# Optimization experiments

Hardware: AMD Instinct MI355X
Metric: run time of the kernel (lower is better)

Reference implementation:

```python
import jax, jax.numpy as jnp
import numpy as np

B = 2          # batch
L = 2048       # seq len
D_MODEL = 1024
D_INNER = 2 * D_MODEL   # expand = 2
D_STATE = 16
D_CONV = 4
DT_RANK = D_MODEL // 16  # 64


def setup_inputs() -> dict:
    key = jax.random.key(0)
    kx, kf, kb = jax.random.split(key, 3)
    d = {"x": jax.random.normal(kx, (B, L, D_MODEL), jnp.float32)}
    for pre, k in (("f_", kf), ("b_", kb)):
        kk = jax.random.split(k, 6)
        d[pre + "in_proj_w"] = jax.random.normal(kk[0], (2 * D_INNER, D_MODEL), jnp.float32) * 0.02
        d[pre + "conv_w"] = jax.random.normal(kk[1], (D_INNER, 1, D_CONV), jnp.float32) * 0.2
        d[pre + "conv_b"] = jnp.zeros((D_INNER,), jnp.float32)
        d[pre + "x_proj_w"] = jax.random.normal(kk[2], (DT_RANK + 2 * D_STATE, D_INNER), jnp.float32) * 0.02
        d[pre + "dt_proj_w"] = jax.random.normal(kk[3], (D_INNER, DT_RANK), jnp.float32) * 0.02
        # dt bias init so softplus(bias) ~ dt in [exp(-4), exp(-2)] range (mamba-style)
        d[pre + "dt_proj_b"] = jax.random.uniform(kk[4], (D_INNER,), jnp.float32, minval=-4.0, maxval=-2.0)
        # S4D-real init: A = -[1..d_state]
        d[pre + "A_log"] = jnp.log(jnp.broadcast_to(jnp.arange(1, D_STATE + 1, dtype=jnp.float32), (D_INNER, D_STATE)))
        d[pre + "D"] = jnp.ones((D_INNER,), jnp.float32)
        d[pre + "out_proj_w"] = jax.random.normal(kk[5], (D_MODEL, D_INNER), jnp.float32) * 0.02
    return d


def _silu(x):
    return x * jax.nn.sigmoid(x)


def _selective_scan(u, dt, A, Bm, Cm, Dp):
    # u, dt: [B, L, d_inner]; Bm, Cm: [B, L, d_state]; A: [d_inner, d_state]; Dp: [d_inner]
    def step(h, inp):
        u_t, dt_t, B_t, C_t = inp                       # [B,d], [B,d], [B,n], [B,n]
        dA = jnp.exp(dt_t[..., None] * A)               # [B, d, n]  (ZOH discretization)
        dBu = dt_t[..., None] * B_t[:, None, :] * u_t[..., None]
        h = dA * h + dBu                                # [B, d, n]
        y = jnp.einsum('bdn,bn->bd', h, C_t)            # [B, d]
        return h, y

    h0 = jnp.zeros((u.shape[0], A.shape[0], A.shape[1]), u.dtype)
    xs = (jnp.swapaxes(u, 0, 1), jnp.swapaxes(dt, 0, 1),
          jnp.swapaxes(Bm, 0, 1), jnp.swapaxes(Cm, 0, 1))
    _, ys = jax.lax.scan(step, h0, xs)                  # ys: [L, B, d_inner]
    return jnp.swapaxes(ys, 0, 1) + u * Dp              # skip connection D*u


def _mamba(x, in_proj_w, conv_w, conv_b, x_proj_w, dt_proj_w, dt_proj_b, A_log, Dp, out_proj_w):
    # x: [B, L, d_model]
    xz = x @ in_proj_w.T                                # [B, L, 2*d_inner]
    xi, z = jnp.split(xz, 2, axis=-1)
    # depthwise causal conv1d, kernel D_CONV, output truncated to L (left pad)
    xc = jax.lax.conv_general_dilated(
        jnp.swapaxes(xi, 1, 2), conv_w, (1,), [(D_CONV - 1, 0)],
        dimension_numbers=('NCH', 'OIH', 'NCH'), feature_group_count=D_INNER)
    xi = _silu(jnp.swapaxes(xc, 1, 2) + conv_b)         # [B, L, d_inner]
    x_dbl = xi @ x_proj_w.T                             # [B, L, dt_rank + 2*d_state]
    dt, Bm, Cm = jnp.split(x_dbl, [DT_RANK, DT_RANK + D_STATE], axis=-1)
    dt = jax.nn.softplus(dt @ dt_proj_w.T + dt_proj_b)  # [B, L, d_inner]
    A = -jnp.exp(A_log)                                 # [d_inner, d_state]
    y = _selective_scan(xi, dt, A, Bm, Cm, Dp)
    y = y * _silu(z)                                    # gated
    return y @ out_proj_w.T                             # [B, L, d_model]


def reference(x,
              f_in_proj_w, f_conv_w, f_conv_b, f_x_proj_w, f_dt_proj_w, f_dt_proj_b, f_A_log, f_D, f_out_proj_w,
              b_in_proj_w, b_conv_w, b_conv_b, b_x_proj_w, b_dt_proj_w, b_dt_proj_b, b_A_log, b_D, b_out_proj_w):
    h_fwd = _mamba(x, f_in_proj_w, f_conv_w, f_conv_b, f_x_proj_w,
                   f_dt_proj_w, f_dt_proj_b, f_A_log, f_D, f_out_proj_w)
    h_bwd = _mamba(jnp.flip(x, axis=1), b_in_proj_w, b_conv_w, b_conv_b, b_x_proj_w,
                   b_dt_proj_w, b_dt_proj_b, b_A_log, b_D, b_out_proj_w)
    h_bwd = jnp.flip(h_bwd, axis=1)
    return jnp.concatenate([h_fwd, h_bwd], axis=-1)     # [B, L, 2*d_model]
```

## Files before the change

### kernel.cpp

```cpp
#include <hip/hip_runtime.h>

#define BB 2
#define LL 2048
#define DM 1024
#define DI 2048
#define NTOK (BB*LL)
#define NC 64
#define CL (LL/NC)
#define NCH (BB*DI)

typedef __bf16 bf16x8 __attribute__((ext_vector_type(8)));
typedef float f32x4 __attribute__((ext_vector_type(4)));
typedef int i32x4 __attribute__((ext_vector_type(4)));

#define LOG2E 1.44269504088896340736f

__device__ __forceinline__ float siluf(float x){ return x / (1.f + __expf(-x)); }
__device__ __forceinline__ float softplusf(float x){
  if (x > 20.f) return x;
  return log1pf(__expf(x));
}
__device__ __forceinline__ unsigned short f2bf(float f){
  unsigned int u = __builtin_bit_cast(unsigned int, f);
  u += 0x7fffu + ((u >> 16) & 1u);
  return (unsigned short)(u >> 16);
}
__device__ __forceinline__ float bf2f(unsigned short u){
  return __builtin_bit_cast(float, (unsigned int)u << 16);
}
template<typename CT>
__device__ __forceinline__ void st_ct(CT* p, float v){
  if constexpr (sizeof(CT)==2) *p = (CT)f2bf(v); else *p = (CT)v;
}

__device__ __forceinline__ void gl_lds16(const unsigned short* g, unsigned short* l){
  __builtin_amdgcn_global_load_lds(
      (const __attribute__((address_space(1))) void*)g,
      (__attribute__((address_space(3))) void*)l, 16, 0, 0);
}

#define SEG0 4096
#define SEG1 8192
#define SEG2 512
#define SEG3 256
#define SEG4 4096
#define CAST_BLOCKS (SEG0+SEG1+SEG2+SEG3+SEG4)

__device__ __forceinline__ void cast4(const float* src, unsigned short* dst){
  float4 v = *reinterpret_cast<const float4*>(src);
  ushort4 o; o.x=f2bf(v.x); o.y=f2bf(v.y); o.z=f2bf(v.z); o.w=f2bf(v.w);
  *reinterpret_cast<ushort4*>(dst) = o;
}

__global__ __launch_bounds__(256) void k_cast_all(
    const float* __restrict__ x,
    const float* __restrict__ ipw0, const float* __restrict__ ipw1,
    const float* __restrict__ xpw0, const float* __restrict__ xpw1,
    const float* __restrict__ dtw0, const float* __restrict__ dtw1,
    const float* __restrict__ opw0, const float* __restrict__ opw1,
    unsigned short* __restrict__ x_bf, unsigned short* __restrict__ w_bf,
    unsigned short* __restrict__ wpad, unsigned short* __restrict__ dtw_bf,
    unsigned short* __restrict__ outw){
  int bid = blockIdx.x;
  int ti = threadIdx.x*4;
  if (bid < SEG0){
    int i = bid*1024 + ti;
    cast4(x + i, x_bf + i);
  } else if (bid < SEG0+SEG1){
    int i = (bid-SEG0)*1024 + ti;
    const int n = (2*DI)*DM;
    const float* src = (i < n) ? ipw0 : ipw1;
    int off = (i < n) ? i : i - n;
    cast4(src + off, w_bf + i);
  } else if (bid < SEG0+SEG1+SEG2){
    int i = (bid-SEG0-SEG1)*1024 + ti;
    const int ntotal = 128*DI, nreal = 96*DI;
    int dir = i / ntotal;
    int r = i - dir*ntotal;
    if (r < nreal){
      cast4((dir ? xpw1 : xpw0) + r, wpad + i);
    } else {
      ushort4 z{0,0,0,0};
      *reinterpret_cast<ushort4*>(wpad + i) = z;
    }
  } else if (bid < SEG0+SEG1+SEG2+SEG3){
    int i = (bid-SEG0-SEG1-SEG2)*1024 + ti;
    const int n = DI*64;
    const float* src = (i < n) ? dtw0 : dtw1;
    int off = (i < n) ? i : i - n;
    cast4(src + off, dtw_bf + i);
  } else {
    int i = (bid-SEG0-SEG1-SEG2-SEG3)*1024 + ti;
    const int n = DM*DI;
    const float* src = (i < n) ? opw0 : opw1;
    int off = (i < n) ? i : i - n;
    cast4(src + off, outw + i);
  }
}

template<int NT>
__global__ __launch_bounds__(512) void k_gemm256(
    const unsigned short* __restrict__ A, int lda,
    const unsigned short* __restrict__ Bw, int ldb, long long bz,
    unsigned short* __restrict__ C, unsigned short* __restrict__ C2, int nsplit,
    int ldc, long long cz){
  __shared__ unsigned short L[2*32768];
  const int dir = blockIdx.z;
  Bw += (size_t)dir*bz;
  const int m0 = blockIdx.y*256;
  const int bn0 = blockIdx.x*256;
  unsigned short* Cout; int n0;
  if (bn0 < nsplit){ Cout = C; n0 = bn0; } else { Cout = C2; n0 = bn0 - nsplit; }
  Cout += (size_t)dir*cz;

  const int tid = threadIdx.x;
  const int w = tid >> 6, lane = tid & 63;
  const int rT = tid >> 3;
  const int sG = (tid & 7) ^ (rT & 7);
  const unsigned short* srcA = A  + (size_t)(m0  + rT)*lda + sG*8;
  const unsigned short* srcB = Bw + (size_t)(bn0 + rT)*ldb + sG*8;
  unsigned short* const lw = &L[w*512];
  const int wmb = (w>>2)*128, wnb = (w&3)*64;
  const int fr = lane & 15;
  const int sK0 = ((lane>>4) ^ (lane&7))*8;

  f32x4 acc[8][4] = {};

  auto STAGE = [&](int kt, int c){
    const unsigned short* a_ = srcA + kt*64;
    const unsigned short* b_ = srcB + kt*64;
    unsigned short* l_ = lw + c*32768;
    gl_lds16(a_,                   l_);
    gl_lds16(a_ + (size_t)64*lda,  l_ + 4096);
    gl_lds16(a_ + (size_t)128*lda, l_ + 8192);
    gl_lds16(a_ + (size_t)192*lda, l_ + 12288);
    gl_lds16(b_,                   l_ + 16384);
    gl_lds16(b_ + (size_t)64*ldb,  l_ + 20480);
    gl_lds16(b_ + (size_t)128*ldb, l_ + 24576);
    gl_lds16(b_ + (size_t)192*ldb, l_ + 28672);
  };
  auto COMPUTE = [&](int c){
    const unsigned short* base = &L[c*32768];
#pragma unroll
    for (int kk=0; kk<2; kk++){
      const int sk = sK0 ^ (kk<<5);
      bf16x8 a[8], b[4];
#pragma unroll
      for (int i=0;i<8;i++)
        a[i] = *reinterpret_cast<const bf16x8*>(&base[(wmb + i*16 + fr)*64 + sk]);
#pragma unroll
      for (int j=0;j<4;j++)
        b[j] = *reinterpret_cast<const bf16x8*>(&base[16384 + (wnb + j*16 + fr)*64 + sk]);
#pragma unroll
      for (int i=0;i<8;i++)
#pragma unroll
        for (int j=0;j<4;j++)
          acc[i][j] = __builtin_amdgcn_mfma_f32_16x16x32_bf16(a[i], b[j], acc[i][j], 0,0,0);
    }
  };

  STAGE(0, 0);
  STAGE(1, 1);
#pragma unroll 2
  for (int t = 0; t < NT-2; ++t){
    asm volatile("s_waitcnt vmcnt(8)" ::: "memory");
    asm volatile("s_barrier" ::: "memory");
    COMPUTE(t & 1);
    asm volatile("s_waitcnt lgkmcnt(0)" ::: "memory");
    asm volatile("s_barrier" ::: "memory");
    STAGE(t+2, t & 1);
  }
  asm volatile("s_waitcnt vmcnt(8)" ::: "memory");
  asm volatile("s_barrier" ::: "memory");
  COMPUTE(NT & 1);
  asm volatile("s_waitcnt vmcnt(0)" ::: "memory");
  asm volatile("s_barrier" ::: "memory");
  COMPUTE((NT-1) & 1);

  const int er = (lane>>4)*4;
#pragma unroll
  for (int i=0;i<8;i++)
#pragma unroll
    for (int j=0;j<4;j++){
      int row = m0 + wmb + i*16 + er;
      int col = n0 + wnb + j*16 + fr;
      unsigned short* cp = Cout + (size_t)row*ldc + col;
#pragma unroll
      for (int r=0;r<4;r++) cp[(size_t)r*ldc] = f2bf(acc[i][j][r]);
    }
}

template<int EPI, int KSPLIT, typename CT>
__global__ __launch_bounds__(256) void k_gemm_bt(
    const unsigned short* __restrict__ A, int lda, long long az,
    const unsigned short* __restrict__ Bw, int ldb, long long bz,
    CT* __restrict__ C, CT* __restrict__ C2, int nsplit,
    int ldc, long long cz, int coffz,
    int K, int coff,
    const float* __restrict__ bias0, const float* __restrict__ bias1){
  __shared__ unsigned short As[128*32];
  __shared__ unsigned short Bs[128*32];
  const int z = blockIdx.z;
  const int dirz = z / KSPLIT, kc = z - dirz*KSPLIT;
  A  += (size_t)dirz*az + (size_t)kc*K;
  Bw += (size_t)dirz*bz + (size_t)kc*K;
  const int bn0 = blockIdx.x*128;
  int n0 = bn0;
  if (bn0 >= nsplit){ C = C2; n0 = bn0 - nsplit; }
  C  += (size_t)z*cz;
  const int co = coff + dirz*coffz;
  const float* bias = dirz ? bias1 : bias0;

  const int t = threadIdx.x;
  const int m0 = blockIdx.y*128;
  const int lane = t & 63, w = t >> 6;
  const int wm = (w>>1)*64, wn = (w&1)*64;

  const int gr = lane >> 2;
  const int gslot = (lane & 3) ^ ((lane >> 3) & 3);
  const unsigned short* gA = A  + (size_t)(m0  + 32*w + gr)*lda + gslot*8;
  const unsigned short* gB = Bw + (size_t)(bn0 + 32*w + gr)*ldb + gslot*8;
  unsigned short* lA = &As[(32*w)*32];
  unsigned short* lB = &Bs[(32*w)*32];

  f32x4 acc[4][4] = {};
  const int fr = lane & 15;
  const int rslot = ((lane>>4) ^ ((lane>>1)&3))*8;

  for (int k0=0; k0<K; k0+=32){
    __syncthreads();
    gl_lds16(gA + k0, lA);
    gl_lds16(gA + (size_t)16*lda + k0, lA + 16*32);
    gl_lds16(gB + k0, lB);
    gl_lds16(gB + (size_t)16*ldb + k0, lB + 16*32);
    __syncthreads();
    bf16x8 af[4], bfr[4];
#pragma unroll
    for (int i=0;i<4;i++){
      af[i]  = *reinterpret_cast<const bf16x8*>(&As[(wm + i*16 + fr)*32 + rslot]);
      bfr[i] = *reinterpret_cast<const bf16x8*>(&Bs[(wn + i*16 + fr)*32 + rslot]);
    }
#pragma unroll
    for (int i=0;i<4;i++)
#pragma unroll
      for (int j=0;j<4;j++)
        acc[i][j] = __builtin_amdgcn_mfma_f32_16x16x32_bf16(af[i], bfr[j], acc[i][j], 0,0,0);
  }
  const int er = (lane>>4)*4;
#pragma unroll
  for (int i=0;i<4;i++)
#pragma unroll
    for (int j=0;j<4;j++){
      int row = m0 + wm + i*16 + er;
      int bcol = n0 + wn + j*16 + fr;
      CT* cp = C + (size_t)row*ldc + co + bcol;
      if (EPI == 1){
        float bv = bias[bcol];
#pragma unroll
        for (int r=0;r<4;r++) st_ct(&cp[(size_t)r*ldc], softplusf(acc[i][j][r] + bv));
      } else {
#pragma unroll
        for (int r=0;r<4;r++) st_ct(&cp[(size_t)r*ldc], acc[i][j][r]);
      }
    }
}

__global__ __launch_bounds__(256) void k_conv_silu(const unsigned short* __restrict__ xpre,
    const float* __restrict__ cw0, const float* __restrict__ cw1,
    const float* __restrict__ cb0, const float* __restrict__ cb1,
    unsigned short* __restrict__ xi_bf){
  const int dir = blockIdx.z;
  const int d0 = threadIdx.x*8;
  const int tok0 = blockIdx.x*4;
  const int b = tok0 >> 11;
  const int t0 = tok0 & (LL-1);
  const float* cw = dir ? cw1 : cw0;
  const float* cb = dir ? cb1 : cb0;
  const unsigned short* xpd = xpre + (size_t)dir*NTOK*DI;
  unsigned short* outp = xi_bf + (size_t)dir*NTOK*DI;

  float wv[4][8];
#pragma unroll
  for (int c=0;c<8;c++){
    float4 w = *reinterpret_cast<const float4*>(cw + (size_t)(d0+c)*4);
    wv[0][c]=w.x; wv[1][c]=w.y; wv[2][c]=w.z; wv[3][c]=w.w;
  }
  float bv[8];
  {
    float4 b0 = *reinterpret_cast<const float4*>(cb + d0);
    float4 b1 = *reinterpret_cast<const float4*>(cb + d0 + 4);
    bv[0]=b0.x; bv[1]=b0.y; bv[2]=b0.z; bv[3]=b0.w;
    bv[4]=b1.x; bv[5]=b1.y; bv[6]=b1.z; bv[7]=b1.w;
  }
  const int rbase = t0 + (dir ? 0 : -3);
  float rows[7][8];
#pragma unroll
  for (int i=0;i<7;i++){
    int r = rbase + i;
    if (r >= 0 && r < LL){
      union { i32x4 v; unsigned short u[8]; } x;
      x.v = *reinterpret_cast<const i32x4*>(xpd + ((size_t)b*LL + r)*DI + d0);
#pragma unroll
      for (int c=0;c<8;c++) rows[i][c] = bf2f(x.u[c]);
    } else {
#pragma unroll
      for (int c=0;c<8;c++) rows[i][c] = 0.f;
    }
  }
#pragma unroll
  for (int j=0;j<4;j++){
    union { i32x4 v; unsigned short u[8]; } o;
#pragma unroll
    for (int c=0;c<8;c++){
      float acc = bv[c];
#pragma unroll
      for (int m=0;m<4;m++){
        float w = dir ? wv[3-m][c] : wv[m][c];
        acc += w * rows[j+m][c];
      }
      o.u[c] = f2bf(siluf(acc));
    }
    *reinterpret_cast<i32x4*>(outp + ((size_t)(tok0+j))*DI + d0) = o.v;
  }
}

__global__ __launch_bounds__(256) void k_xred(const float* __restrict__ part,
    float* __restrict__ xdbl, unsigned short* __restrict__ xdbl_bf){
  int idx = blockIdx.x*256 + threadIdx.x;
  if (idx >= 2*NTOK*96) return;
  int dir = idx / (NTOK*96);
  int rem = idx - dir*(NTOK*96);
  int tok = rem / 96, j = rem - tok*96;
  const float* pd = part + (size_t)dir*4*NTOK*128;
  const size_t czs = (size_t)NTOK*128;
  size_t o = (size_t)tok*128 + j;
  float v = pd[o] + pd[czs + o] + pd[2*czs + o] + pd[3*czs + o];
  xdbl[(size_t)dir*NTOK*96 + (size_t)tok*96 + j] = v;
  if (j < 64) xdbl_bf[(size_t)dir*NTOK*64 + (size_t)tok*64 + j] = f2bf(v);
}

__device__ __forceinline__ void powtree(float q, float* dA){
  dA[0]=q;
  dA[1]=dA[0]*dA[0];
  dA[2]=dA[1]*dA[0];
  dA[3]=dA[1]*dA[1];
  dA[4]=dA[3]*dA[0];
  dA[5]=dA[3]*dA[1];
  dA[6]=dA[3]*dA[2];
  dA[7]=dA[3]*dA[3];
#pragma unroll
  for (int n=8;n<16;n++) dA[n]=dA[7]*dA[n-8];
}
__device__ __forceinline__ bool chk_struct(const float* Alog2){
  bool ok = true;
  float a0 = Alog2[0];
#pragma unroll
  for (int n=1;n<16;n++){
    float e = a0*(float)(n+1);
    ok = ok && (fabsf(Alog2[n]-e) <= 1e-5f*fabsf(e) + 1e-12f);
  }
  return ok;
}

__global__ __launch_bounds__(256) void k_scan_p1(const unsigned short* __restrict__ u,
    const unsigned short* __restrict__ dt, const float* __restrict__ xdbl,
    const float* __restrict__ A_log0, const float* __restrict__ A_log1,
    float* __restrict__ hloc, float* __restrict__ dtsum){
  __shared__ float Bs[CL*16];
  const int dir = blockIdx.z;
  u    += (size_t)dir*NTOK*DI;
  dt   += (size_t)dir*NTOK*DI;
  xdbl += (size_t)dir*NTOK*96;
  const float* A_log = dir ? A_log1 : A_log0;
  const int tid = threadIdx.x;
  const int ch = blockIdx.x*256 + tid;
  const int c = blockIdx.y;
  const int b = (blockIdx.x*256) >> 11;
  const int d = ch & (DI-1);
  for (int i = tid; i < CL*16; i += 256){
    int s = i >> 4, j = i & 15;
    int sg = c*CL + s;
    int tt = dir ? (LL-1-sg) : sg;
    Bs[i] = xdbl[((size_t)b*LL + tt)*96 + 64 + j];
  }
  float Alog2[16];
  {
    const float4* ap = reinterpret_cast<const float4*>(A_log + (size_t)d*16);
#pragma unroll
    for (int q=0;q<4;q++){
      float4 v = ap[q];
      Alog2[q*4+0] = -__expf(v.x)*LOG2E;
      Alog2[q*4+1] = -__expf(v.y)*LOG2E;
      Alog2[q*4+2] = -__expf(v.z)*LOG2E;
      Alog2[q*4+3] = -__expf(v.w)*LOG2E;
    }
  }
  const bool structured = chk_struct(Alog2);
  __syncthreads();
  float h[16];
#pragma unroll
  for (int n=0;n<16;n++) h[n]=0.f;
  float dts = 0.f;
  int tok0 = b*LL + (dir ? (LL-1-c*CL) : c*CL);
  const unsigned short* up = u + (size_t)tok0*DI + d;
  const unsigned short* dtp = dt + (size_t)tok0*DI + d;
  const ptrdiff_t stp = dir ? -(ptrdiff_t)DI : (ptrdiff_t)DI;
  if (structured){
    const float a0 = Alog2[0];
#pragma unroll 2
    for (int s=0; s<CL; s++){
      float uv  = bf2f(*up); up += stp;
      float dtv = bf2f(*dtp); dtp += stp;
      float dtu = dtv*uv;
      dts += dtv;
      const f32x4* br = reinterpret_cast<const f32x4*>(&Bs[s*16]);
      f32x4 B0=br[0], B1=br[1], B2=br[2], B3=br[3];
      float dA[16];
      powtree(__builtin_amdgcn_exp2f(dtv*a0), dA);
#pragma unroll
      for (int n=0;n<16;n++){
        float Bv = (n<4)?B0[n&3] : (n<8)?B1[n&3] : (n<12)?B2[n&3] : B3[n&3];
        h[n] = dA[n]*h[n] + dtu*Bv;
      }
    }
  } else {
#pragma unroll 2
    for (int s=0; s<CL; s++){
      float uv  = bf2f(*up); up += stp;
      float dtv = bf2f(*dtp); dtp += stp;
      float dtu = dtv*uv;
      dts += dtv;
      const f32x4* br = reinterpret_cast<const f32x4*>(&Bs[s*16]);
      f32x4 B0=br[0], B1=br[1], B2=br[2], B3=br[3];
#pragma unroll
      for (int n=0;n<16;n++){
        float dA = __builtin_amdgcn_exp2f(dtv*Alog2[n]);
        float Bv = (n<4)?B0[n&3] : (n<8)?B1[n&3] : (n<12)?B2[n&3] : B3[n&3];
        h[n] = dA*h[n] + dtu*Bv;
      }
    }
  }
  float* hp = hloc + (((size_t)(dir*NC + c)*NCH + ch))*16;
#pragma unroll
  for (int q=0;q<4;q++)
    *reinterpret_cast<f32x4*>(hp + q*4) = f32x4{h[q*4],h[q*4+1],h[q*4+2],h[q*4+3]};
  dtsum[(size_t)(dir*NC + c)*NCH + ch] = dts;
}

__global__ __launch_bounds__(256) void k_scan_comb(float* __restrict__ hloc,
    const float* __restrict__ dtsum,
    const float* __restrict__ A_log0, const float* __restrict__ A_log1){
  int i = blockIdx.x*256 + threadIdx.x;
  int dir = i / (NCH*16);
  int j = i - dir*(NCH*16);
  int ch = j >> 4, n = j & 15;
  int d = ch & (DI-1);
  const float* A_log = dir ? A_log1 : A_log0;
  float Alog2 = -__expf(A_log[(size_t)d*16 + n])*LOG2E;
  float hs = 0.f;
#pragma unroll 4
  for (int c=0; c<NC; c++){
    size_t base = (size_t)(dir*NC + c)*NCH + ch;
    float pa = __builtin_amdgcn_exp2f(dtsum[base]*Alog2);
    size_t idx = base*16 + n;
    float h = hloc[idx];
    hloc[idx] = hs;
    hs = pa*hs + h;
  }
}

__global__ __launch_bounds__(256) void k_scan_p2(unsigned short* __restrict__ uy,
    const unsigned short* __restrict__ dt, const float* __restrict__ xdbl,
    const unsigned short* __restrict__ zbuf,
    const float* __restrict__ A_log0, const float* __restrict__ A_log1,
    const float* __restrict__ Dp0, const float* __restrict__ Dp1,
    const float* __restrict__ hstart){
  __shared__ float BCs[CL*32];
  const int dir = blockIdx.z;
  uy   += (size_t)dir*NTOK*DI;
  dt   += (size_t)dir*NTOK*DI;
  zbuf += (size_t)dir*NTOK*DI;
  xdbl += (size_t)dir*NTOK*96;
  const float* A_log = dir ? A_log1 : A_log0;
  const float* Dp = dir ? Dp1 : Dp0;
  const int tid = threadIdx.x;
  const int ch = blockIdx.x*256 + tid;
  const int c = blockIdx.y;
  const int b = (blockIdx.x*256) >> 11;
  const int d = ch & (DI-1);
  for (int i = tid; i < CL*32; i += 256){
    int s = i >> 5, j = i & 31;
    int sg = c*CL + s;
    int tt = dir ? (LL-1-sg) : sg;
    BCs[i] = xdbl[((size_t)b*LL + tt)*96 + 64 + j];
  }
  float Alog2[16];
  {
    const float4* ap = reinterpret_cast<const float4*>(A_log + (size_t)d*16);
#pragma unroll
    for (int q=0;q<4;q++){
      float4 v = ap[q];
      Alog2[q*4+0] = -__expf(v.x)*LOG2E;
      Alog2[q*4+1] = -__expf(v.y)*LOG2E;
      Alog2[q*4+2] = -__expf(v.z)*LOG2E;
      Alog2[q*4+3] = -__expf(v.w)*LOG2E;
    }
  }
  const bool structured = chk_struct(Alog2);
  float h[16];
  {
    const float* hp = hstart + (((size_t)(dir*NC + c)*NCH + ch))*16;
#pragma unroll
    for (int q=0;q<4;q++){
      f32x4 v = *reinterpret_cast<const f32x4*>(hp + q*4);
      h[q*4]=v[0]; h[q*4+1]=v[1]; h[q*4+2]=v[2]; h[q*4+3]=v[3];
    }
  }
  const float Dval = Dp[d];
  __syncthreads();
  int tok0 = b*LL + (dir ? (LL-1-c*CL) : c*CL);
  unsigned short* up = uy + (size_t)tok0*DI + d;
  const unsigned short* zp = zbuf + (size_t)tok0*DI + d;
  const unsigned short* dtp = dt + (size_t)tok0*DI + d;
  const ptrdiff_t stp = dir ? -(ptrdiff_t)DI : (ptrdiff_t)DI;
  if (structured){
    const float a0 = Alog2[0];
#pragma unroll 2
    for (int s=0; s<CL; s++){
      float uv  = bf2f(*up);
      float zv  = bf2f(*zp); zp += stp;
      float dtv = bf2f(*dtp); dtp += stp;
      float dtu = dtv*uv;
      float y = Dval*uv;
      const f32x4* br = reinterpret_cast<const f32x4*>(&BCs[s*32]);
      f32x4 B0=br[0], B1=br[1], B2=br[2], B3=br[3];
      f32x4 C0=br[4], C1=br[5], C2=br[6], C3=br[7];
      float dA[16];
      powtree(__builtin_amdgcn_exp2f(dtv*a0), dA);
#pragma unroll
      for (int n=0;n<16;n++){
        float Bv = (n<4)?B0[n&3] : (n<8)?B1[n&3] : (n<12)?B2[n&3] : B3[n&3];
        float Cv = (n<4)?C0[n&3] : (n<8)?C1[n&3] : (n<12)?C2[n&3] : C3[n&3];
        h[n] = dA[n]*h[n] + dtu*Bv;
        y += h[n]*Cv;
      }
      *up = f2bf(y * siluf(zv)); up += stp;
    }
  } else {
#pragma unroll 2
    for (int s=0; s<CL; s++){
      float uv  = bf2f(*up);
      float zv  = bf2f(*zp); zp += stp;
      float dtv = bf2f(*dtp); dtp += stp;
      float dtu = dtv*uv;
      float y = Dval*uv;
      const f32x4* br = reinterpret_cast<const f32x4*>(&BCs[s*32]);
      f32x4 B0=br[0], B1=br[1], B2=br[2], B3=br[3];
      f32x4 C0=br[4], C1=br[5], C2=br[6], C3=br[7];
#pragma unroll
      for (int n=0;n<16;n++){
        float dA = __builtin_amdgcn_exp2f(dtv*Alog2[n]);
        float Bv = (n<4)?B0[n&3] : (n<8)?B1[n&3] : (n<12)?B2[n&3] : B3[n&3];
        float Cv = (n<4)?C0[n&3] : (n<8)?C1[n&3] : (n<12)?C2[n&3] : C3[n&3];
        h[n] = dA*h[n] + dtu*Bv;
        y += h[n]*Cv;
      }
      *up = f2bf(y * siluf(zv)); up += stp;
    }
  }
}

extern "C" void kernel_launch(void* const* d_in, const int* in_sizes, int n_in,
                              void* d_out, int out_size, void* d_ws, size_t ws_size,
                              hipStream_t stream){
  (void)in_sizes; (void)n_in; (void)out_size; (void)ws_size;
  const float* x = (const float*)d_in[0];
  const float* ipw[2], *cw[2], *cb[2], *xpw[2], *dtw_[2], *dtb[2], *Alog[2], *Dp[2], *opw[2];
  for (int dir=0; dir<2; dir++){
    ipw[dir]  = (const float*)d_in[1 + dir*9 + 0];
    cw[dir]   = (const float*)d_in[1 + dir*9 + 1];
    cb[dir]   = (const float*)d_in[1 + dir*9 + 2];
    xpw[dir]  = (const float*)d_in[1 + dir*9 + 3];
    dtw_[dir] = (const float*)d_in[1 + dir*9 + 4];
    dtb[dir]  = (const float*)d_in[1 + dir*9 + 5];
    Alog[dir] = (const float*)d_in[1 + dir*9 + 6];
    Dp[dir]   = (const float*)d_in[1 + dir*9 + 7];
    opw[dir]  = (const float*)d_in[1 + dir*9 + 8];
  }
  char* p = (char*)d_ws;
  auto alloc = [&](size_t bytes)->void*{ void* r=(void*)p; p += (bytes+255)&~(size_t)255; return r; };
  unsigned short* x_bf   = (unsigned short*)alloc((size_t)NTOK*DM*2);
  unsigned short* w_bf   = (unsigned short*)alloc((size_t)2*(2*DI)*DM*2);
  float* part            = (float*)w_bf;
  unsigned short* xpre   = (unsigned short*)alloc((size_t)2*NTOK*DI*2);
  unsigned short* zbuf   = (unsigned short*)alloc((size_t)2*NTOK*DI*2);
  unsigned short* xi_bf  = (unsigned short*)alloc((size_t)2*NTOK*DI*2);
  float* xdbl            = (float*)alloc((size_t)2*NTOK*96*4);
  unsigned short* xdbl_bf= (unsigned short*)alloc((size_t)2*NTOK*64*2);
  unsigned short* dt_bf  = (unsigned short*)alloc((size_t)2*NTOK*DI*2);
  unsigned short* wpad   = (unsigned short*)alloc((size_t)2*128*DI*2);
  unsigned short* dtw_bf = (unsigned short*)alloc((size_t)2*DI*64*2);
  unsigned short* outw   = (unsigned short*)alloc((size_t)2*DM*DI*2);
  float* hloc  = (float*)d_ws;
  float* dtsum = (float*)((char*)d_ws + (size_t)32*1024*1024);

  k_cast_all<<<CAST_BLOCKS, 256, 0, stream>>>(
      x, ipw[0], ipw[1], xpw[0], xpw[1], dtw_[0], dtw_[1], opw[0], opw[1],
      x_bf, w_bf, wpad, dtw_bf, outw);

  k_gemm256<16><<<dim3(16,16,2), 512, 0, stream>>>(
      x_bf, DM, w_bf, DM, (long long)(2*DI)*DM,
      xpre, zbuf, DI, DI, (long long)NTOK*DI);
  k_conv_silu<<<dim3(NTOK/4,1,2), 256, 0, stream>>>(xpre, cw[0], cw[1], cb[0], cb[1], xi_bf);
  k_gemm_bt<0,4,float><<<dim3(1,32,8), 256, 0, stream>>>(
      xi_bf, DI, (long long)NTOK*DI, wpad, DI, (long long)128*DI,
      part, part, 1<<30, 128, (long long)NTOK*128, 0, 512, 0, nullptr, nullptr);
  k_xred<<<(2*NTOK*96+255)/256, 256, 0, stream>>>(part, xdbl, xdbl_bf);
  k_gemm_bt<1,1,unsigned short><<<dim3(16,32,2), 256, 0, stream>>>(
      xdbl_bf, 64, (long long)NTOK*64, dtw_bf, 64, (long long)DI*64,
      dt_bf, dt_bf, 1<<30, DI, (long long)NTOK*DI, 0, 64, 0, dtb[0], dtb[1]);
  k_scan_p1<<<dim3(NCH/256, NC, 2), 256, 0, stream>>>(xi_bf, dt_bf, xdbl,
      Alog[0], Alog[1], hloc, dtsum);
  k_scan_comb<<<2*NCH*16/256, 256, 0, stream>>>(hloc, dtsum, Alog[0], Alog[1]);
  k_scan_p2<<<dim3(NCH/256, NC, 2), 256, 0, stream>>>(xi_bf, dt_bf, xdbl, zbuf,
      Alog[0], Alog[1], Dp[0], Dp[1], hloc);
  k_gemm_bt<0,1,float><<<dim3(8,32,2), 256, 0, stream>>>(
      xi_bf, DI, (long long)NTOK*DI, outw, DI, (long long)DM*DI,
      (float*)d_out, (float*)d_out, 1<<30, 2*DM, 0, DM, DI, 0, nullptr, nullptr);
}
```

Baseline: 353.4 us.

## Restructure GEMM pipelines into half-K stages with prefetch and triple buffering

The 256x256 GEMM now splits each 64-wide K tile into two 32-wide halves. The next tile's half is issued into the other buffer before computing the current half, and MFMA bursts are wrapped in s_setprio. The smaller k_gemm_bt kernel drops its two-syncthreads-per-iteration loop for a three-stage ring buffer that prefetches two tiles ahead with vmcnt waits and one barrier per step. Both aim to overlap global-to-LDS loads with MFMA work and cut barrier stalls, at the cost of more LDS in the small GEMM and tighter waitcnt correctness reasoning.

```diff
diff --git a/kernel.cpp b/kernel.cpp
--- a/kernel.cpp
+++ b/kernel.cpp
@@ -104,7 +104,7 @@
     const unsigned short* __restrict__ Bw, int ldb, long long bz,
     unsigned short* __restrict__ C, unsigned short* __restrict__ C2, int nsplit,
     int ldc, long long cz){
-  __shared__ unsigned short L[2*32768];
+  __shared__ unsigned short L[65536];
   const int dir = blockIdx.z;
   Bw += (size_t)dir*bz;
   const int m0 = blockIdx.y*256;
@@ -115,67 +115,75 @@
 
   const int tid = threadIdx.x;
   const int w = tid >> 6, lane = tid & 63;
-  const int rT = tid >> 3;
-  const int sG = (tid & 7) ^ (rT & 7);
+  const int rT = tid >> 2;
+  const int sG = (tid & 3) ^ ((tid >> 3) & 3);
   const unsigned short* srcA = A  + (size_t)(m0  + rT)*lda + sG*8;
   const unsigned short* srcB = Bw + (size_t)(bn0 + rT)*ldb + sG*8;
   unsigned short* const lw = &L[w*512];
   const int wmb = (w>>2)*128, wnb = (w&3)*64;
   const int fr = lane & 15;
-  const int sK0 = ((lane>>4) ^ (lane&7))*8;
+  const int sk = ((lane>>4) ^ ((fr>>1)&3))*8;
 
   f32x4 acc[8][4] = {};
 
-  auto STAGE = [&](int kt, int c){
-    const unsigned short* a_ = srcA + kt*64;
-    const unsigned short* b_ = srcB + kt*64;
-    unsigned short* l_ = lw + c*32768;
+  auto STAGE = [&](int kt, int kk, int c){
+    const unsigned short* a_ = srcA + kt*64 + kk*32;
+    const unsigned short* b_ = srcB + kt*64 + kk*32;
+    unsigned short* l_ = lw + c*32768 + kk*16384;
     gl_lds16(a_,                   l_);
-    gl_lds16(a_ + (size_t)64*lda,  l_ + 4096);
-    gl_lds16(a_ + (size_t)128*lda, l_ + 8192);
-    gl_lds16(a_ + (size_t)192*lda, l_ + 12288);
-    gl_lds16(b_,                   l_ + 16384);
-    gl_lds16(b_ + (size_t)64*ldb,  l_ + 20480);
-    gl_lds16(b_ + (size_t)128*ldb, l_ + 24576);
-    gl_lds16(b_ + (size_t)192*ldb, l_ + 28672);
+    gl_lds16(a_ + (size_t)128*lda, l_ + 4096);
+    gl_lds16(b_,                   l_ + 8192);
+    gl_lds16(b_ + (size_t)128*ldb, l_ + 12288);
   };
-  auto COMPUTE = [&](int c){
-    const unsigned short* base = &L[c*32768];
-#pragma unroll
-    for (int kk=0; kk<2; kk++){
-      const int sk = sK0 ^ (kk<<5);
-      bf16x8 a[8], b[4];
-#pragma unroll
-      for (int i=0;i<8;i++)
-        a[i] = *reinterpret_cast<const bf16x8*>(&base[(wmb + i*16 + fr)*64 + sk]);
-#pragma unroll
-      for (int j=0;j<4;j++)
-        b[j] = *reinterpret_cast<const bf16x8*>(&base[16384 + (wnb + j*16 + fr)*64 + sk]);
-#pragma unroll
-      for (int i=0;i<8;i++)
-#pragma unroll
-        for (int j=0;j<4;j++)
-          acc[i][j] = __builtin_amdgcn_mfma_f32_16x16x32_bf16(a[i], b[j], acc[i][j], 0,0,0);
-    }
+
+  auto HALF = [&](int c, int kk, bool stage, int kt){
+    if (stage) STAGE(kt, kk, c^1);
+    const unsigned short* base = &L[c*32768 + kk*16384];
+    bf16x8 a[8];
+#pragma unroll
+    for (int i=0;i<8;i++)
+      a[i] = *reinterpret_cast<const bf16x8*>(&base[(wmb + i*16 + fr)*32 + sk]);
+    bf16x8 b0 = *reinterpret_cast<const bf16x8*>(&base[8192 + (wnb +  0 + fr)*32 + sk]);
+    bf16x8 b1 = *reinterpret_cast<const bf16x8*>(&base[8192 + (wnb + 16 + fr)*32 + sk]);
+    __builtin_amdgcn_s_setprio(1);
+#pragma unroll
+    for (int i=0;i<8;i++){
+      acc[i][0] = __builtin_amdgcn_mfma_f32_16x16x32_bf16(a[i], b0, acc[i][0], 0,0,0);
+      acc[i][1] = __builtin_amdgcn_mfma_f32_16x16x32_bf16(a[i], b1, acc[i][1], 0,0,0);
+    }
+    __builtin_amdgcn_s_setprio(0);
+    bf16x8 b2 = *reinterpret_cast<const bf16x8*>(&base[8192 + (wnb + 32 + fr)*32 + sk]);
+    bf16x8 b3 = *reinterpret_cast<const bf16x8*>(&base[8192 + (wnb + 48 + fr)*32 + sk]);
+    __builtin_amdgcn_s_setprio(1);
+#pragma unroll
+    for (int i=0;i<8;i++){
+      acc[i][2] = __builtin_amdgcn_mfma_f32_16x16x32_bf16(a[i], b2, acc[i][2], 0,0,0);
+      acc[i][3] = __builtin_amdgcn_mfma_f32_16x16x32_bf16(a[i], b3, acc[i][3], 0,0,0);
+    }
+    __builtin_amdgcn_s_setprio(0);
   };
 
-  STAGE(0, 0);
-  STAGE(1, 1);
+  STAGE(0, 0, 0);
+  STAGE(0, 1, 0);
 #pragma unroll 2
-  for (int t = 0; t < NT-2; ++t){
-    asm volatile("s_waitcnt vmcnt(8)" ::: "memory");
+  for (int t = 0; t < NT-1; ++t){
+    const int c = t & 1;
+    asm volatile("s_waitcnt vmcnt(4)" ::: "memory");
     asm volatile("s_barrier" ::: "memory");
-    COMPUTE(t & 1);
-    asm volatile("s_waitcnt lgkmcnt(0)" ::: "memory");
+    HALF(c, 0, true, t+1);
+    asm volatile("s_waitcnt vmcnt(4)" ::: "memory");
     asm volatile("s_barrier" ::: "memory");
-    STAGE(t+2, t & 1);
-  }
-  asm volatile("s_waitcnt vmcnt(8)" ::: "memory");
-  asm volatile("s_barrier" ::: "memory");
-  COMPUTE(NT & 1);
-  asm volatile("s_waitcnt vmcnt(0)" ::: "memory");
-  asm volatile("s_barrier" ::: "memory");
-  COMPUTE((NT-1) & 1);
+    HALF(c, 1, true, t+1);
+  }
+  {
+    const int c = (NT-1) & 1;
+    asm volatile("s_waitcnt vmcnt(4)" ::: "memory");
+    asm volatile("s_barrier" ::: "memory");
+    HALF(c, 0, false, 0);
+    asm volatile("s_waitcnt vmcnt(0)" ::: "memory");
+    asm volatile("s_barrier" ::: "memory");
+    HALF(c, 1, false, 0);
+  }
 
   const int er = (lane>>4)*4;
 #pragma unroll
@@ -198,8 +206,8 @@
     int ldc, long long cz, int coffz,
     int K, int coff,
     const float* __restrict__ bias0, const float* __restrict__ bias1){
-  __shared__ unsigned short As[128*32];
-  __shared__ unsigned short Bs[128*32];
+  __shared__ unsigned short As[3*128*32];
+  __shared__ unsigned short Bs[3*128*32];
   const int z = blockIdx.z;
   const int dirz = z / KSPLIT, kc = z - dirz*KSPLIT;
   A  += (size_t)dirz*az + (size_t)kc*K;
@@ -227,24 +235,34 @@
   const int fr = lane & 15;
   const int rslot = ((lane>>4) ^ ((lane>>1)&3))*8;
 
-  for (int k0=0; k0<K; k0+=32){
-    __syncthreads();
-    gl_lds16(gA + k0, lA);
-    gl_lds16(gA + (size_t)16*lda + k0, lA + 16*32);
-    gl_lds16(gB + k0, lB);
-    gl_lds16(gB + (size_t)16*ldb + k0, lB + 16*32);
-    __syncthreads();
+  const int NTk = K >> 5;
+  auto STG = [&](int kt, int c){
+    gl_lds16(gA + kt*32, lA + c*4096);
+    gl_lds16(gA + (size_t)16*lda + kt*32, lA + c*4096 + 16*32);
+    gl_lds16(gB + kt*32, lB + c*4096);
+    gl_lds16(gB + (size_t)16*ldb + kt*32, lB + c*4096 + 16*32);
+  };
+  STG(0, 0);
+  if (NTk > 1) STG(1, 1);
+  int c = 0, cs = 2;
+  for (int kt = 0; kt < NTk; ++kt){
+    if (kt < NTk-1){ asm volatile("s_waitcnt vmcnt(4)" ::: "memory"); }
+    else           { asm volatile("s_waitcnt vmcnt(0)" ::: "memory"); }
+    asm volatile("s_barrier" ::: "memory");
+    if (kt+2 < NTk) STG(kt+2, cs);
     bf16x8 af[4], bfr[4];
 #pragma unroll
     for (int i=0;i<4;i++){
-      af[i]  = *reinterpret_cast<const bf16x8*>(&As[(wm + i*16 + fr)*32 + rslot]);
-      bfr[i] = *reinterpret_cast<const bf16x8*>(&Bs[(wn + i*16 + fr)*32 + rslot]);
+      af[i]  = *reinterpret_cast<const bf16x8*>(&As[c*4096 + (wm + i*16 + fr)*32 + rslot]);
+      bfr[i] = *reinterpret_cast<const bf16x8*>(&Bs[c*4096 + (wn + i*16 + fr)*32 + rslot]);
     }
 #pragma unroll
     for (int i=0;i<4;i++)
 #pragma unroll
       for (int j=0;j<4;j++)
         acc[i][j] = __builtin_amdgcn_mfma_f32_16x16x32_bf16(af[i], bfr[j], acc[i][j], 0,0,0);
+    c = (c==2) ? 0 : c+1;
+    cs = (cs==2) ? 0 : cs+1;
   }
   const int er = (lane>>4)*4;
 #pragma unroll
```

Measured after the change: 364.3 us. 1.03x slower.
